# Optimization experiments

Hardware: AMD Instinct MI355X
Metric: run time of the kernel (lower is better)

The kernel has to match this reference:

```python
import jax, jax.numpy as jnp
import numpy as np

NEG = -9e15
N_NODES, IN_DIM, H1, H2, HEADS, DEC, N_EDGES, B_PAIRS = 4096, 512, 256, 128, 4, 512, 131072, 4096


def setup_inputs() -> dict:
    key = jax.random.key(0)
    ks = jax.random.split(key, 24)
    d = {}
    d["x_o"] = jax.random.normal(ks[0], (N_NODES, IN_DIM), jnp.float32)
    d["x_a"] = jax.random.normal(ks[1], (N_NODES, IN_DIM), jnp.float32)
    d["edge_index"] = jax.random.randint(ks[2], (2, N_EDGES), 0, N_NODES)
    d["idx"] = jax.random.randint(ks[3], (2, B_PAIRS), 0, N_NODES)
    # GAT layer 1 (in=IN_DIM, out=H1), per-head stacked params
    d["W1"] = jax.random.normal(ks[4], (HEADS, IN_DIM, H1)) * (IN_DIM ** -0.5)
    d["a1"] = jax.random.normal(ks[5], (HEADS, 2 * H1)) * 0.1
    d["lin1"] = jax.random.normal(ks[6], (HEADS * H1, H1)) * ((HEADS * H1) ** -0.5)
    d["res1"] = jax.random.normal(ks[7], (IN_DIM, H1)) * (IN_DIM ** -0.5)
    # GAT layer 2 (in=H1, out=H2)
    d["W2"] = jax.random.normal(ks[8], (HEADS, H1, H2)) * (H1 ** -0.5)
    d["a2"] = jax.random.normal(ks[9], (HEADS, 2 * H2)) * 0.1
    d["lin2"] = jax.random.normal(ks[10], (HEADS * H2, H2)) * ((HEADS * H2) ** -0.5)
    d["res2"] = jax.random.normal(ks[11], (H1, H2)) * (H1 ** -0.5)
    # heads
    d["mlp1_w"] = jax.random.normal(ks[12], (H2, H2)) * (H2 ** -0.5)
    d["mlp1_b"] = jnp.zeros((H2,))
    d["disc_w"] = jax.random.normal(ks[13], (H2, H2)) * (H2 ** -0.5)
    d["disc_b"] = jnp.zeros(())
    d["dec1_w"] = jax.random.normal(ks[14], (2 * H2, DEC)) * ((2 * H2) ** -0.5)
    d["dec1_b"] = jnp.zeros((DEC,))
    d["dec2_w"] = jax.random.normal(ks[15], (DEC, 1)) * (DEC ** -0.5)
    d["dec2_b"] = jnp.zeros((1,))
    d["adv_w"] = jax.random.normal(ks[16], (H2, H2)) * (H2 ** -0.5)
    d["adv_b"] = jnp.zeros((H2,))
    return d


def _gat_residual_layer(h, mask, W, a, lin, res):
    # W: [H, Fin, Fo], a: [H, 2*Fo]. e_ij = leakyrelu(Wh_i . a[:Fo] + Wh_j . a[Fo:])
    # (algebraically identical to the NxN all-pairs concat @ a in the torch code).
    def head(Wk, ak):
        Wh = h @ Wk                      # [N, Fo]
        Fo = Wk.shape[1]
        src = Wh @ ak[:Fo]               # [N]
        dst = Wh @ ak[Fo:]               # [N]
        e = jax.nn.leaky_relu(src[:, None] + dst[None, :], 0.2)  # [N, N]
        att = jax.nn.softmax(jnp.where(mask, e, NEG), axis=1)
        return jax.nn.elu(att @ Wh)      # [N, Fo]

    heads = jax.vmap(head)(W, a)         # [H, N, Fo]
    Hn, N, Fo = heads.shape
    concat = jnp.transpose(heads, (1, 0, 2)).reshape(N, Hn * Fo)
    mh = jax.nn.elu(concat @ lin)
    return jax.nn.relu(mh + h @ res)     # relu(relu(x)) == relu(x); dropout off in eval


def reference(x_o, x_a, W1, a1, lin1, res1, W2, a2, lin2, res2,
              mlp1_w, mlp1_b, disc_w, disc_b, dec1_w, dec1_b,
              dec2_w, dec2_b, adv_w, adv_b, edge_index, idx):
    N = x_o.shape[0]
    mask = jnp.zeros((N, N), jnp.bool_).at[edge_index[0], edge_index[1]].set(True)

    def encode(x):
        h = _gat_residual_layer(x, mask, W1, a1, lin1, res1)
        h = _gat_residual_layer(h, mask, W2, a2, lin2, res2)
        return h

    x2_o = encode(x_o)                   # [N, H2]
    x2_o_a = encode(x_a)

    h_os = jax.nn.sigmoid(x2_o.mean(0)) @ mlp1_w + mlp1_b      # [H2]
    h_os_a = jax.nn.sigmoid(x2_o_a.mean(0)) @ mlp1_w + mlp1_b

    def disc(c, h_pl, h_mi):  # Bilinear(h, c) with out=1
        sc1 = (h_pl @ disc_w) @ c + disc_b
        sc2 = (h_mi @ disc_w) @ c + disc_b
        return jnp.stack([sc1, sc2], axis=1)                    # [N, 2]

    ret_os = disc(h_os, x2_o, x2_o_a)
    ret_os_a = disc(h_os_a, x2_o_a, x2_o)

    # extract_entities, default branch (task_type not in {LDA, MDA, LMI})
    entity1 = x2_o[idx[0]]
    entity2 = x2_o[idx[1]]
    z = jnp.concatenate([entity1, entity2], axis=1)             # [B, 2*H2]
    hdec = jax.nn.relu(z @ dec1_w + dec1_b)
    log1 = hdec @ dec2_w + dec2_b                               # [B, 1]
    log = jax.nn.sigmoid(log1)

    sc_1 = (x2_o @ adv_w + adv_b).sum(1)[None, :]               # [1, N]
    sc_2 = (x2_o_a @ adv_w + adv_b).sum(1)[None, :]
    logits = jnp.concatenate([sc_1, sc_2], axis=1)              # [1, 2N]

    return (log, ret_os, ret_os_a, x2_o, logits, log1)
```

## Files before the change

kernel.cpp:

```cpp
#include <hip/hip_runtime.h>
#include <stdint.h>

#define N_NODES 4096
#define N_EDGES 131072

typedef __attribute__((ext_vector_type(8))) short short8;
typedef __attribute__((ext_vector_type(4))) float floatx4;

__device__ __forceinline__ float bf2f(unsigned short u) {
  union { unsigned u; float f; } v; v.u = ((unsigned)u) << 16; return v.f;
}
__device__ __forceinline__ unsigned short f2bf(float f) {
  union { float f; unsigned u; } v; v.f = f;
  unsigned r = 0x7FFFu + ((v.u >> 16) & 1u);
  return (unsigned short)((v.u + r) >> 16);
}
__device__ __forceinline__ float wredsum(float x) {
#pragma unroll
  for (int d = 32; d >= 1; d >>= 1) x += __shfl_xor(x, d);
  return x;
}
__device__ __forceinline__ float wredmax(float x) {
#pragma unroll
  for (int d = 32; d >= 1; d >>= 1) x = fmaxf(x, __shfl_xor(x, d));
  return x;
}
__device__ __forceinline__ void gload16(const void* g, void* l) {
  __builtin_amdgcn_global_load_lds(
      (const __attribute__((address_space(1))) unsigned*)g,
      (__attribute__((address_space(3))) unsigned*)l, 16, 0, 0);
}

__global__ __launch_bounds__(256) void gemm128(
    const unsigned short* __restrict__ A, const unsigned short* __restrict__ Bt,
    int M, int N, int K, unsigned short* __restrict__ Cb,
    const float* __restrict__ avec, float* __restrict__ sdv, int FO) {
  __shared__ __align__(16) unsigned short As[128 * 32];
  __shared__ __align__(16) unsigned short Bs[128 * 32];
  const int t = threadIdx.x, lane = t & 63, w = t >> 6;
  const int wr = w >> 1, wc = w & 1;
  const int n0 = blockIdx.x * 128, m0 = blockIdx.y * 128;
  floatx4 acc[4][4] = {};
  const int arow = t >> 2;
  const int schunk = (t & 3) ^ ((arow >> 1) & 3);

  for (int kt = 0; kt < K; kt += 32) {
    __syncthreads();
    gload16(A + (size_t)(m0 + arow) * K + kt + schunk * 8, &As[t * 8]);
    gload16(A + (size_t)(m0 + 64 + arow) * K + kt + schunk * 8, &As[(256 + t) * 8]);
    gload16(Bt + (size_t)(n0 + arow) * K + kt + schunk * 8, &Bs[t * 8]);
    gload16(Bt + (size_t)(n0 + 64 + arow) * K + kt + schunk * 8, &Bs[(256 + t) * 8]);
    __syncthreads();
    short8 af[4], bfr[4];
    const int koff = lane >> 4;
#pragma unroll
    for (int m = 0; m < 4; ++m) {
      const int r = wr * 64 + (lane & 15) + m * 16;
      af[m] = *(const short8*)&As[r * 32 + ((koff ^ ((r >> 1) & 3)) << 3)];
    }
#pragma unroll
    for (int n = 0; n < 4; ++n) {
      const int r = wc * 64 + (lane & 15) + n * 16;
      bfr[n] = *(const short8*)&Bs[r * 32 + ((koff ^ ((r >> 1) & 3)) << 3)];
    }
#pragma unroll
    for (int m = 0; m < 4; ++m)
#pragma unroll
      for (int n = 0; n < 4; ++n)
        acc[m][n] = __builtin_amdgcn_mfma_f32_16x16x32_bf16(af[m], bfr[n], acc[m][n], 0, 0, 0);
  }

  const int rb = m0 + wr * 64 + (lane >> 4) * 4;
  const int cb = n0 + wc * 64 + (lane & 15);
#pragma unroll
  for (int m = 0; m < 4; ++m)
#pragma unroll
    for (int n = 0; n < 4; ++n) {
      const int col = cb + n * 16;
#pragma unroll
      for (int r = 0; r < 4; ++r) {
        const int row = rb + m * 16 + r;
        Cb[(size_t)row * N + col] = f2bf(acc[m][n][r]);
      }
    }

  if (avec) {
    const int h = n0 / FO;
    const int cw0 = cb - h * FO;
    float as_[4], ad_[4];
#pragma unroll
    for (int n = 0; n < 4; ++n) {
      as_[n] = avec[h * 2 * FO + cw0 + n * 16];
      ad_[n] = avec[h * 2 * FO + FO + cw0 + n * 16];
    }
#pragma unroll
    for (int m = 0; m < 4; ++m)
#pragma unroll
      for (int r = 0; r < 4; ++r) {
        float sp = 0.f, dp = 0.f;
#pragma unroll
        for (int n = 0; n < 4; ++n) {
          sp += acc[m][n][r] * as_[n];
          dp += acc[m][n][r] * ad_[n];
        }
#pragma unroll
        for (int d = 1; d < 16; d <<= 1) {
          sp += __shfl_xor(sp, d);
          dp += __shfl_xor(dp, d);
        }
        if ((lane & 15) == 0) {
          const int row = rb + m * 16 + r;
          atomicAdd(&sdv[row * 8 + h], sp);
          atomicAdd(&sdv[row * 8 + 4 + h], dp);
        }
      }
  }
}

__device__ __forceinline__ void stage64(const unsigned short* __restrict__ G,
                                        unsigned short* lds, int row0, int K,
                                        int kt, int t) {
  const int l0 = t, l1 = t + 256;
  const int r0 = l0 >> 3, c0 = l0 & 7;
  const int r1 = l1 >> 3, c1 = l1 & 7;
  gload16(G + (size_t)(row0 + r0) * K + kt + ((c0 ^ (r0 & 7)) << 3), &lds[l0 * 8]);
  gload16(G + (size_t)(row0 + r1) * K + kt + ((c1 ^ (r1 & 7)) << 3), &lds[l1 * 8]);
}
__device__ __forceinline__ short8 frag64(const unsigned short* lds, int r, int c) {
  return *(const short8*)&lds[r * 64 + ((c ^ (r & 7)) << 3)];
}

template <int EP>
__global__ __launch_bounds__(256) void gemm64(
    const unsigned short* __restrict__ A, const unsigned short* __restrict__ Bt,
    int M, int N, int K, unsigned short* __restrict__ Cb,
    const float* __restrict__ bias) {
  __shared__ __align__(16) unsigned short As[64 * 64];
  __shared__ __align__(16) unsigned short Bs[64 * 64];
  const int t = threadIdx.x, lane = t & 63, w = t >> 6;
  const int wr = w >> 1, wc = w & 1;
  const int n0 = blockIdx.x * 64, m0 = blockIdx.y * 64;
  floatx4 acc[2][2] = {};

  for (int kt = 0; kt < K; kt += 64) {
    __syncthreads();
    stage64(A, As, m0, K, kt, t);
    stage64(Bt, Bs, n0, K, kt, t);
    __syncthreads();
    short8 af[2][2], bfv[2][2];
#pragma unroll
    for (int m = 0; m < 2; ++m) {
      const int ra = wr * 32 + (lane & 15) + m * 16;
#pragma unroll
      for (int kk = 0; kk < 2; ++kk)
        af[m][kk] = frag64(As, ra, (lane >> 4) + kk * 4);
    }
#pragma unroll
    for (int n = 0; n < 2; ++n) {
      const int rb = wc * 32 + (lane & 15) + n * 16;
#pragma unroll
      for (int kk = 0; kk < 2; ++kk)
        bfv[n][kk] = frag64(Bs, rb, (lane >> 4) + kk * 4);
    }
#pragma unroll
    for (int kk = 0; kk < 2; ++kk)
#pragma unroll
      for (int m = 0; m < 2; ++m)
#pragma unroll
        for (int n = 0; n < 2; ++n)
          acc[m][n] = __builtin_amdgcn_mfma_f32_16x16x32_bf16(af[m][kk], bfv[n][kk], acc[m][n], 0, 0, 0);
  }

  const int rb = m0 + wr * 32 + (lane >> 4) * 4;
  const int cb = n0 + wc * 32 + (lane & 15);
#pragma unroll
  for (int m = 0; m < 2; ++m)
#pragma unroll
    for (int n = 0; n < 2; ++n) {
      const int col = cb + n * 16;
#pragma unroll
      for (int r = 0; r < 4; ++r) {
        const int row = rb + m * 16 + r;
        float v = acc[m][n][r];
        if (EP == 4) { v += bias[col]; v = v > 0.f ? v : 0.f; }
        Cb[(size_t)row * N + col] = f2bf(v);
      }
    }
}

template <int EP>
__global__ __launch_bounds__(256) void gemm64dual(
    const unsigned short* __restrict__ A1, const unsigned short* __restrict__ B1t, int K1,
    const unsigned short* __restrict__ A2, const unsigned short* __restrict__ B2t, int K2,
    int N, unsigned short* __restrict__ Cb,
    float* __restrict__ Cfo, float* __restrict__ Cfa) {
  __shared__ __align__(16) unsigned short As[64 * 64];
  __shared__ __align__(16) unsigned short Bs[64 * 64];
  const int t = threadIdx.x, lane = t & 63, w = t >> 6;
  const int wr = w >> 1, wc = w & 1;
  const int n0 = blockIdx.x * 64, m0 = blockIdx.y * 64;
  floatx4 acc[2][2] = {};

#pragma unroll 1
  for (int pass = 0; pass < 2; ++pass) {
    const unsigned short* A = pass ? A2 : A1;
    const unsigned short* Bt = pass ? B2t : B1t;
    const int K = pass ? K2 : K1;
    for (int kt = 0; kt < K; kt += 64) {
      __syncthreads();
      stage64(A, As, m0, K, kt, t);
      stage64(Bt, Bs, n0, K, kt, t);
      __syncthreads();
      short8 af[2][2], bfv[2][2];
#pragma unroll
      for (int m = 0; m < 2; ++m) {
        const int ra = wr * 32 + (lane & 15) + m * 16;
#pragma unroll
        for (int kk = 0; kk < 2; ++kk)
          af[m][kk] = frag64(As, ra, (lane >> 4) + kk * 4);
      }
#pragma unroll
      for (int n = 0; n < 2; ++n) {
        const int rb = wc * 32 + (lane & 15) + n * 16;
#pragma unroll
        for (int kk = 0; kk < 2; ++kk)
          bfv[n][kk] = frag64(Bs, rb, (lane >> 4) + kk * 4);
      }
#pragma unroll
      for (int kk = 0; kk < 2; ++kk)
#pragma unroll
        for (int m = 0; m < 2; ++m)
#pragma unroll
          for (int n = 0; n < 2; ++n)
            acc[m][n] = __builtin_amdgcn_mfma_f32_16x16x32_bf16(af[m][kk], bfv[n][kk], acc[m][n], 0, 0, 0);
    }
    if (pass == 0) {
#pragma unroll
      for (int m = 0; m < 2; ++m)
#pragma unroll
        for (int n = 0; n < 2; ++n)
#pragma unroll
          for (int r = 0; r < 4; ++r) {
            float v = acc[m][n][r];
            acc[m][n][r] = v > 0.f ? v : expm1f(v);
          }
    }
  }

  const int rb = m0 + wr * 32 + (lane >> 4) * 4;
  const int cb = n0 + wc * 32 + (lane & 15);
#pragma unroll
  for (int m = 0; m < 2; ++m)
#pragma unroll
    for (int n = 0; n < 2; ++n) {
      const int col = cb + n * 16;
#pragma unroll
      for (int r = 0; r < 4; ++r) {
        const int row = rb + m * 16 + r;
        float v = acc[m][n][r];
        v = v > 0.f ? v : 0.f;
        if (EP == 0) {
          Cb[(size_t)row * N + col] = f2bf(v);
        } else {
          float* bb = (row < 4096) ? Cfo : Cfa;
          bb[(size_t)(row & 4095) * N + col] = v;
        }
      }
    }
}

__global__ __launch_bounds__(256) void scatter_kernel(
    const int* __restrict__ ei, unsigned long long* __restrict__ mb,
    float* __restrict__ sd1, float* __restrict__ sd2) {
  int b = blockIdx.x;
  if (b < 512) {
    int e = b * 256 + threadIdx.x;
    int r = ei[e], c = ei[N_EDGES + e];
    atomicOr(&mb[(size_t)r * 64 + (c >> 6)], 1ull << (c & 63));
  } else {
    int z = (b - 512) * 256 + threadIdx.x;
    if (z < 65536) sd1[z] = 0.f;
    else sd2[z - 65536] = 0.f;
  }
}

__global__ __launch_bounds__(256) void pack2_kernel(
    const float* W1, const float* lin1, const float* res1, const float* W2,
    const float* lin2, const float* res2, const float* dec1,
    const float* xo, const float* xa,
    unsigned short* dW1, unsigned short* dlin1, unsigned short* dres1,
    unsigned short* dW2, unsigned short* dlin2, unsigned short* dres2,
    unsigned short* ddec1, unsigned short* x16) {
  const int b = blockIdx.x, t = threadIdx.x;
  if (b >= 1248) {
    int ib = b - 1248;
    const float* src = (ib < 512) ? xo : xa;
    unsigned short* dst = x16 + ((ib < 512) ? 0 : (size_t)4096 * 512);
    size_t base = (size_t)(ib & 511) * 4096;
#pragma unroll
    for (int q = 0; q < 4; ++q) {
      size_t o = base + q * 1024 + t * 4;
      float4 v = *(const float4*)&src[o];
      ushort4 u = {f2bf(v.x), f2bf(v.y), f2bf(v.z), f2bf(v.w)};
      *(ushort4*)&dst[o] = u;
    }
    return;
  }
  const float* src; unsigned short* dst; int K, F, nFt, tb;
  if (b < 512)       { int h = b >> 7;        src = W1 + h * 131072; dst = dW1 + h * 131072; K = 512;  F = 256; nFt = 8;  tb = b & 127; }
  else if (b < 768)  {                        src = lin1;            dst = dlin1;            K = 1024; F = 256; nFt = 8;  tb = b - 512; }
  else if (b < 896)  {                        src = res1;            dst = dres1;            K = 512;  F = 256; nFt = 8;  tb = b - 768; }
  else if (b < 1024) { int h = (b - 896) >> 5; src = W2 + h * 32768; dst = dW2 + h * 32768;  K = 256;  F = 128; nFt = 4;  tb = (b - 896) & 31; }
  else if (b < 1088) {                        src = lin2;            dst = dlin2;            K = 512;  F = 128; nFt = 4;  tb = b - 1024; }
  else if (b < 1120) {                        src = res2;            dst = dres2;            K = 256;  F = 128; nFt = 4;  tb = b - 1088; }
  else               {                        src = dec1;            dst = ddec1;            K = 256;  F = 512; nFt = 16; tb = b - 1120; }
  const int k0 = (tb / nFt) * 32, f0 = (tb % nFt) * 32;
  __shared__ float tile[32][33];
  {
    int r = t >> 3, c4 = (t & 7) * 4;
    float4 v = *(const float4*)&src[(size_t)(k0 + r) * F + f0 + c4];
    tile[r][c4] = v.x; tile[r][c4 + 1] = v.y; tile[r][c4 + 2] = v.z; tile[r][c4 + 3] = v.w;
  }
  __syncthreads();
  {
    int f = t >> 3, k4 = (t & 7) * 4;
    ushort4 u;
    u.x = f2bf(tile[k4 + 0][f]); u.y = f2bf(tile[k4 + 1][f]);
    u.z = f2bf(tile[k4 + 2][f]); u.w = f2bf(tile[k4 + 3][f]);
    *(ushort4*)&dst[(size_t)(f0 + f) * K + k0 + k4] = u;
  }
}

template <int FO>
__global__ __launch_bounds__(256) void attn_kernel(
    const unsigned long long* __restrict__ mb, const float* __restrict__ sd,
    const unsigned short* __restrict__ Wh, unsigned short* __restrict__ outp) {
  constexpr int E = FO / 64;
  constexpr int W = 4 * FO;
  constexpr int WGCAP = 512;
  __shared__ __align__(16) char smem[8208 + 8320];
  unsigned short* nbr = (unsigned short*)smem;
  float (*wgs)[520] = (float (*)[520])(smem + 8208);
  float* red = (float*)smem;
  __shared__ int s_cnt;
  __shared__ float s_inv[4];
  const int i = blockIdx.x;
  const int mrow = i & 4095;
  const int base = i & ~4095;
  const int t = threadIdx.x;
  const int lane = t & 63, wv = t >> 6;

  if (t < 64) {
    unsigned long long wb = mb[(size_t)mrow * 64 + t];
    int pc = __popcll(wb);
    int inc = pc;
#pragma unroll
    for (int d = 1; d < 64; d <<= 1) {
      int v = __shfl_up(inc, d);
      if (t >= d) inc += v;
    }
    if (t == 63) s_cnt = inc;
    int off = inc - pc;
    while (wb) {
      int b = __builtin_ctzll(wb);
      nbr[off++] = (unsigned short)(t * 64 + b);
      wb &= wb - 1;
    }
  }
  __syncthreads();
  const int cnt = s_cnt;

  if (cnt == 0) {
    const float wg = 1.f / 4096.f;
    float acc0[E] = {};
    for (int j = 0; j < N_NODES; ++j) {
      const unsigned short* p = Wh + (size_t)(base + j) * W + wv * FO + lane * E;
#pragma unroll
      for (int q = 0; q < E; ++q) acc0[q] += wg * bf2f(p[q]);
    }
    unsigned short* op = outp + (size_t)i * W + wv * FO + lane * E;
#pragma unroll
    for (int q = 0; q < E; ++q) {
      float v = acc0[q];
      op[q] = f2bf(v > 0.f ? v : expm1f(v));
    }
    return;
  }

  if (t < 8) nbr[(cnt + t < 4103) ? cnt + t : 4103] = 0;
  const float src_i = sd[(size_t)i * 8 + wv];
  float m = -1e30f;
  for (int nn = lane; nn < cnt; nn += 64) {
    int j = base + nbr[nn];
    float x = src_i + sd[(size_t)j * 8 + 4 + wv];
    m = fmaxf(m, x > 0.f ? x : 0.2f * x);
  }
  m = wredmax(m);
  float ssum = 0.f;
  for (int nn = lane; nn < cnt; nn += 64) {
    int j = base + nbr[nn];
    float x = src_i + sd[(size_t)j * 8 + 4 + wv];
    float e = x > 0.f ? x : 0.2f * x;
    float g = __expf(e - m);
    if (nn < WGCAP) wgs[wv][nn] = g;
    ssum += g;
  }
  ssum = wredsum(ssum);
  if (lane == 0) s_inv[wv] = 1.f / ssum;
  if (lane < 8) wgs[wv][(cnt < WGCAP ? cnt : WGCAP) + lane] = 0.f;
  __syncthreads();

  float acc[4][E] = {};
  const int lim = cnt < WGCAP ? cnt : WGCAP;
  const int ngroups = (lim + 7) >> 3;
  for (int g = wv; g < ngroups; g += 4) {
    const int nn = g * 8;
    ushort4 ja = *(const ushort4*)&nbr[nn];
    ushort4 jb = *(const ushort4*)&nbr[nn + 4];
    const int js[8] = {ja.x, ja.y, ja.z, ja.w, jb.x, jb.y, jb.z, jb.w};
#pragma unroll
    for (int h = 0; h < 4; ++h) {
      float4 wa = *(const float4*)&wgs[h][nn];
      float4 wb4 = *(const float4*)&wgs[h][nn + 4];
      const float ws[8] = {wa.x, wa.y, wa.z, wa.w, wb4.x, wb4.y, wb4.z, wb4.w};
      if constexpr (E == 4) {
        uint2 r[8];
#pragma unroll
        for (int q = 0; q < 8; ++q)
          r[q] = *(const uint2*)(Wh + (size_t)(base + js[q]) * W + h * FO + lane * E);
#pragma unroll
        for (int q = 0; q < 8; ++q) {
          acc[h][0] += ws[q] * bf2f((unsigned short)(r[q].x & 0xffff));
          acc[h][1] += ws[q] * bf2f((unsigned short)(r[q].x >> 16));
          acc[h][2] += ws[q] * bf2f((unsigned short)(r[q].y & 0xffff));
          acc[h][3] += ws[q] * bf2f((unsigned short)(r[q].y >> 16));
        }
      } else {
        unsigned r[8];
#pragma unroll
        for (int q = 0; q < 8; ++q)
          r[q] = *(const unsigned*)(Wh + (size_t)(base + js[q]) * W + h * FO + lane * E);
#pragma unroll
        for (int q = 0; q < 8; ++q) {
          acc[h][0] += ws[q] * bf2f((unsigned short)(r[q] & 0xffff));
          acc[h][1] += ws[q] * bf2f((unsigned short)(r[q] >> 16));
        }
      }
    }
  }
  for (int nn = WGCAP; nn < cnt; ++nn) {
    int j = base + nbr[nn];
    float x = src_i + sd[(size_t)j * 8 + 4 + wv];
    float e = x > 0.f ? x : 0.2f * x;
    float g = __expf(e - m);
    const unsigned short* p = Wh + (size_t)j * W + wv * FO + lane * E;
#pragma unroll
    for (int q = 0; q < E; ++q) acc[wv][q] += g * bf2f(p[q]);
  }
  __syncthreads();
#pragma unroll
  for (int h = 0; h < 4; ++h)
#pragma unroll
    for (int q = 0; q < E; ++q)
      red[(wv * 4 + h) * 64 * E + lane * E + q] = acc[h][q];
  __syncthreads();
  float fin[E] = {};
#pragma unroll
  for (int w2 = 0; w2 < 4; ++w2)
#pragma unroll
    for (int q = 0; q < E; ++q)
      fin[q] += red[(w2 * 4 + wv) * 64 * E + lane * E + q];
  const float inv = s_inv[wv];
  unsigned short* op = outp + (size_t)i * W + wv * FO + lane * E;
#pragma unroll
  for (int q = 0; q < E; ++q) {
    float v = fin[q] * inv;
    op[q] = f2bf(v > 0.f ? v : expm1f(v));
  }
}

__global__ __launch_bounds__(128) void colsum_kernel(
    const float* __restrict__ x2o, const float* __restrict__ x2a,
    float* __restrict__ small) {
  int b = blockIdx.x, f = threadIdx.x;
  const float* x = (b < 64) ? x2o : x2a;
  float* s = (b < 64) ? small : (small + 128);
  int r0 = (b & 63) * 64;
  float acc = 0.f;
  for (int r = 0; r < 64; ++r) acc += x[(size_t)(r0 + r) * 128 + f];
  atomicAdd(&s[f], acc);
}

__global__ __launch_bounds__(128) void finalize_kernel(
    float* __restrict__ small, const float* __restrict__ mlp1_w,
    const float* __restrict__ mlp1_b, const float* __restrict__ disc_w,
    const float* __restrict__ adv_w, const float* __restrict__ adv_b) {
  __shared__ float so[128], sa[128], ho[128], ha[128];
  int f = threadIdx.x;
  so[f] = 1.f / (1.f + __expf(-small[f] * (1.f / 4096.f)));
  sa[f] = 1.f / (1.f + __expf(-small[128 + f] * (1.f / 4096.f)));
  __syncthreads();
  float aco = mlp1_b[f], aca = mlp1_b[f];
  for (int c = 0; c < 128; ++c) {
    aco += so[c] * mlp1_w[c * 128 + f];
    aca += sa[c] * mlp1_w[c * 128 + f];
  }
  ho[f] = aco;
  ha[f] = aca;
  __syncthreads();
  float vo = 0.f, va = 0.f, ar = 0.f;
  for (int c = 0; c < 128; ++c) {
    vo += disc_w[f * 128 + c] * ho[c];
    va += disc_w[f * 128 + c] * ha[c];
    ar += adv_w[f * 128 + c];
  }
  small[256 + f] = vo;
  small[384 + f] = va;
  small[512 + f] = ar;
  if (f == 0) {
    float b = 0.f;
    for (int c = 0; c < 128; ++c) b += adv_b[c];
    small[640] = b;
  }
}

__global__ __launch_bounds__(256) void pernode_kernel(
    const float* __restrict__ x2o, const float* __restrict__ x2a,
    const float* __restrict__ small, const float* __restrict__ disc_b,
    float* __restrict__ out) {
  const float* v_os = small + 256;
  const float* v_a = small + 384;
  const float* adv_rs = small + 512;
  int lane = threadIdx.x & 63, wv = threadIdx.x >> 6;
  int i = blockIdx.x * 4 + wv;
  float2 xo = *(const float2*)&x2o[(size_t)i * 128 + lane * 2];
  float2 xa = *(const float2*)&x2a[(size_t)i * 128 + lane * 2];
  float2 vo = *(const float2*)&v_os[lane * 2];
  float2 va = *(const float2*)&v_a[lane * 2];
  float2 ar = *(const float2*)&adv_rs[lane * 2];
  float poo = wredsum(xo.x * vo.x + xo.y * vo.y);
  float pao = wredsum(xa.x * vo.x + xa.y * vo.y);
  float paa = wredsum(xa.x * va.x + xa.y * va.y);
  float poa = wredsum(xo.x * va.x + xo.y * va.y);
  float pov = wredsum(xo.x * ar.x + xo.y * ar.y);
  float pav = wredsum(xa.x * ar.x + xa.y * ar.y);
  if (lane == 0) {
    float db = disc_b[0], bv = small[640];
    out[4096 + 2 * i] = poo + db;
    out[4096 + 2 * i + 1] = pao + db;
    out[12288 + 2 * i] = paa + db;
    out[12288 + 2 * i + 1] = poa + db;
    out[544768 + i] = pov + bv;
    out[548864 + i] = pav + bv;
  }
}

__global__ __launch_bounds__(256) void gather_kernel(
    const float* __restrict__ x2o, const int* __restrict__ idx,
    unsigned short* __restrict__ z) {
  int i = blockIdx.x, c = threadIdx.x;
  int s = (c < 128) ? idx[i] : idx[4096 + i];
  z[(size_t)i * 256 + c] = f2bf(x2o[(size_t)s * 128 + (c & 127)]);
}

__global__ __launch_bounds__(256) void dec2_kernel(
    const unsigned short* __restrict__ hdec, const float* __restrict__ w2,
    const float* __restrict__ b2, float* __restrict__ out) {
  int lane = threadIdx.x & 63, wv = threadIdx.x >> 6;
  int i = blockIdx.x * 4 + wv;
  float s = 0.f;
#pragma unroll
  for (int q = 0; q < 8; ++q) {
    int f = lane + q * 64;
    s += bf2f(hdec[(size_t)i * 512 + f]) * w2[f];
  }
  s = wredsum(s);
  if (lane == 0) {
    float v = s + b2[0];
    out[552960 + i] = v;
    out[i] = 1.f / (1.f + __expf(-v));
  }
}

extern "C" void kernel_launch(void* const* d_in, const int* in_sizes, int n_in,
                              void* d_out, int out_size, void* d_ws, size_t ws_size,
                              hipStream_t stream) {
  const float* x_o = (const float*)d_in[0];
  const float* x_a = (const float*)d_in[1];
  const int* ei = (const int*)d_in[2];
  const int* idx = (const int*)d_in[3];
  const float* W1 = (const float*)d_in[4];
  const float* a1 = (const float*)d_in[5];
  const float* lin1 = (const float*)d_in[6];
  const float* res1 = (const float*)d_in[7];
  const float* W2 = (const float*)d_in[8];
  const float* a2 = (const float*)d_in[9];
  const float* lin2 = (const float*)d_in[10];
  const float* res2 = (const float*)d_in[11];
  const float* mlp1_w = (const float*)d_in[12];
  const float* mlp1_b = (const float*)d_in[13];
  const float* disc_w = (const float*)d_in[14];
  const float* disc_b = (const float*)d_in[15];
  const float* dec1_w = (const float*)d_in[16];
  const float* dec1_b = (const float*)d_in[17];
  const float* dec2_w = (const float*)d_in[18];
  const float* dec2_b = (const float*)d_in[19];
  const float* adv_w = (const float*)d_in[20];
  const float* adv_b = (const float*)d_in[21];
  float* out = (float*)d_out;

  char* w = (char*)d_ws;
  size_t off = 0;
  auto alloc = [&](size_t b) {
    char* p = w + off;
    off += (b + 255) & ~(size_t)255;
    return p;
  };
  unsigned long long* mb = (unsigned long long*)alloc((size_t)4096 * 64 * 8);
  unsigned short* x16 = (unsigned short*)alloc((size_t)8192 * 512 * 2);
  unsigned short* Wh1 = (unsigned short*)alloc((size_t)8192 * 1024 * 2);
  unsigned short* ho1 = (unsigned short*)alloc((size_t)8192 * 1024 * 2);
  unsigned short* h1 = (unsigned short*)alloc((size_t)8192 * 256 * 2);
  unsigned short* Wh2 = (unsigned short*)alloc((size_t)8192 * 512 * 2);
  unsigned short* ho2 = (unsigned short*)alloc((size_t)8192 * 512 * 2);
  float* x2a = (float*)alloc((size_t)4096 * 128 * 4);
  float* sd1 = (float*)alloc((size_t)8192 * 8 * 4);
  float* sd2 = (float*)alloc((size_t)8192 * 8 * 4);
  float* small = (float*)alloc(1024 * 4);
  unsigned short* tW1 = (unsigned short*)alloc((size_t)524288 * 2);
  unsigned short* tlin1 = (unsigned short*)alloc((size_t)262144 * 2);
  unsigned short* tres1 = (unsigned short*)alloc((size_t)131072 * 2);
  unsigned short* tW2 = (unsigned short*)alloc((size_t)131072 * 2);
  unsigned short* tlin2 = (unsigned short*)alloc((size_t)65536 * 2);
  unsigned short* tres2 = (unsigned short*)alloc((size_t)32768 * 2);
  unsigned short* tdec1 = (unsigned short*)alloc((size_t)131072 * 2);
  unsigned short* z16 = (unsigned short*)alloc((size_t)4096 * 256 * 2);
  unsigned short* hdec = (unsigned short*)alloc((size_t)4096 * 512 * 2);

  hipMemsetAsync(mb, 0, (size_t)4096 * 64 * 8, stream);
  hipMemsetAsync(small, 0, 1024, stream);
  scatter_kernel<<<1024, 256, 0, stream>>>(ei, mb, sd1, sd2);
  pack2_kernel<<<2272, 256, 0, stream>>>(W1, lin1, res1, W2, lin2, res2, dec1_w,
                                         x_o, x_a, tW1, tlin1, tres1, tW2,
                                         tlin2, tres2, tdec1, x16);

  float* x2o_out = out + 20480;

  gemm128<<<dim3(8, 64), 256, 0, stream>>>(x16, tW1, 8192, 1024, 512, Wh1, a1, sd1, 256);
  attn_kernel<256><<<8192, 256, 0, stream>>>(mb, sd1, Wh1, ho1);
  gemm64dual<0><<<dim3(4, 128), 256, 0, stream>>>(ho1, tlin1, 1024, x16, tres1, 512, 256, h1, nullptr, nullptr);
  gemm128<<<dim3(4, 64), 256, 0, stream>>>(h1, tW2, 8192, 512, 256, Wh2, a2, sd2, 128);
  attn_kernel<128><<<8192, 256, 0, stream>>>(mb, sd2, Wh2, ho2);
  gemm64dual<1><<<dim3(2, 128), 256, 0, stream>>>(ho2, tlin2, 512, h1, tres2, 256, 128, nullptr, x2o_out, x2a);

  colsum_kernel<<<128, 128, 0, stream>>>(x2o_out, x2a, small);
  finalize_kernel<<<1, 128, 0, stream>>>(small, mlp1_w, mlp1_b, disc_w, adv_w, adv_b);
  pernode_kernel<<<1024, 256, 0, stream>>>(x2o_out, x2a, small, disc_b, out);
  gather_kernel<<<4096, 256, 0, stream>>>(x2o_out, idx, z16);
  gemm64<4><<<dim3(8, 64), 256, 0, stream>>>(z16, tdec1, 4096, 512, 256, hdec, dec1_b);
  dec2_kernel<<<1024, 256, 0, stream>>>(hdec, dec2_w, dec2_b, out);
}
```

Baseline: 232.6 us.

## Precompute CSR neighbor lists and remap attention to one wave per row-head

Adds three kernels that build a global CSR neighbor list (count, scan, fill) from the adjacency bitmask once, so the two attention layers no longer decode the bitmask per block. The attention kernel now gives each wave its own (row, head) pair, and the 8 combos of head and encoder are interleaved across blocks. This removes the cross-wave shared-memory reduction and two barriers. In exchange it adds three small launches, including a single-wave serial scan, and each wave now walks its full neighbor list alone instead of splitting the list across the block.

```diff
diff --git a/kernel.cpp b/kernel.cpp
--- a/kernel.cpp
+++ b/kernel.cpp
@@ -281,6 +281,54 @@
     int z = (b - 512) * 256 + threadIdx.x;
     if (z < 65536) sd1[z] = 0.f;
     else sd2[z - 65536] = 0.f;
+  }
+}
+
+__global__ __launch_bounds__(256) void csr_count(
+    const unsigned long long* __restrict__ mb, int* __restrict__ rcnt) {
+  int r = blockIdx.x * 256 + threadIdx.x;
+  int c = 0;
+#pragma unroll 8
+  for (int w = 0; w < 64; ++w) c += __popcll(mb[(size_t)r * 64 + w]);
+  rcnt[r] = c;
+}
+
+__global__ __launch_bounds__(64) void csr_scan(
+    const int* __restrict__ rcnt, int* __restrict__ rbase) {
+  int l = threadIdx.x;
+  int s = 0;
+  for (int k = 0; k < 64; ++k) s += rcnt[l * 64 + k];
+  int pre = s;
+#pragma unroll
+  for (int d = 1; d < 64; d <<= 1) {
+    int v = __shfl_up(pre, d);
+    if (l >= d) pre += v;
+  }
+  pre -= s;
+  int run = pre;
+  for (int k = 0; k < 64; ++k) {
+    rbase[l * 64 + k] = run;
+    run += rcnt[l * 64 + k];
+  }
+}
+
+__global__ __launch_bounds__(64) void csr_fill(
+    const unsigned long long* __restrict__ mb, const int* __restrict__ rbase,
+    unsigned short* __restrict__ nbrg) {
+  int r = blockIdx.x, t = threadIdx.x;
+  unsigned long long wb = mb[(size_t)r * 64 + t];
+  int pc = __popcll(wb);
+  int inc = pc;
+#pragma unroll
+  for (int d = 1; d < 64; d <<= 1) {
+    int v = __shfl_up(inc, d);
+    if (t >= d) inc += v;
+  }
+  int off = rbase[r] + inc - pc;
+  while (wb) {
+    int b = __builtin_ctzll(wb);
+    nbrg[off++] = (unsigned short)(t * 64 + b);
+    wb &= wb - 1;
   }
 }
 
@@ -332,149 +380,103 @@
 }
 
 template <int FO>
-__global__ __launch_bounds__(256) void attn_kernel(
-    const unsigned long long* __restrict__ mb, const float* __restrict__ sd,
+__global__ __launch_bounds__(256) void attn2_kernel(
+    const int* __restrict__ rcnt, const int* __restrict__ rbase,
+    const unsigned short* __restrict__ nbrg, const float* __restrict__ sd,
     const unsigned short* __restrict__ Wh, unsigned short* __restrict__ outp) {
   constexpr int E = FO / 64;
   constexpr int W = 4 * FO;
-  constexpr int WGCAP = 512;
-  __shared__ __align__(16) char smem[8208 + 8320];
-  unsigned short* nbr = (unsigned short*)smem;
-  float (*wgs)[520] = (float (*)[520])(smem + 8208);
-  float* red = (float*)smem;
-  __shared__ int s_cnt;
-  __shared__ float s_inv[4];
-  const int i = blockIdx.x;
-  const int mrow = i & 4095;
-  const int base = i & ~4095;
-  const int t = threadIdx.x;
-  const int lane = t & 63, wv = t >> 6;
-
-  if (t < 64) {
-    unsigned long long wb = mb[(size_t)mrow * 64 + t];
-    int pc = __popcll(wb);
-    int inc = pc;
-#pragma unroll
-    for (int d = 1; d < 64; d <<= 1) {
-      int v = __shfl_up(inc, d);
-      if (t >= d) inc += v;
-    }
-    if (t == 63) s_cnt = inc;
-    int off = inc - pc;
-    while (wb) {
-      int b = __builtin_ctzll(wb);
-      nbr[off++] = (unsigned short)(t * 64 + b);
-      wb &= wb - 1;
-    }
-  }
-  __syncthreads();
-  const int cnt = s_cnt;
-
-  if (cnt == 0) {
-    const float wg = 1.f / 4096.f;
-    float acc0[E] = {};
-    for (int j = 0; j < N_NODES; ++j) {
-      const unsigned short* p = Wh + (size_t)(base + j) * W + wv * FO + lane * E;
-#pragma unroll
-      for (int q = 0; q < E; ++q) acc0[q] += wg * bf2f(p[q]);
-    }
-    unsigned short* op = outp + (size_t)i * W + wv * FO + lane * E;
-#pragma unroll
-    for (int q = 0; q < E; ++q) {
-      float v = acc0[q];
-      op[q] = f2bf(v > 0.f ? v : expm1f(v));
-    }
-    return;
-  }
-
-  if (t < 8) nbr[(cnt + t < 4103) ? cnt + t : 4103] = 0;
-  const float src_i = sd[(size_t)i * 8 + wv];
-  float m = -1e30f;
-  for (int nn = lane; nn < cnt; nn += 64) {
-    int j = base + nbr[nn];
-    float x = src_i + sd[(size_t)j * 8 + 4 + wv];
-    m = fmaxf(m, x > 0.f ? x : 0.2f * x);
-  }
-  m = wredmax(m);
-  float ssum = 0.f;
-  for (int nn = lane; nn < cnt; nn += 64) {
-    int j = base + nbr[nn];
-    float x = src_i + sd[(size_t)j * 8 + 4 + wv];
-    float e = x > 0.f ? x : 0.2f * x;
-    float g = __expf(e - m);
-    if (nn < WGCAP) wgs[wv][nn] = g;
-    ssum += g;
-  }
-  ssum = wredsum(ssum);
-  if (lane == 0) s_inv[wv] = 1.f / ssum;
-  if (lane < 8) wgs[wv][(cnt < WGCAP ? cnt : WGCAP) + lane] = 0.f;
-  __syncthreads();
-
-  float acc[4][E] = {};
-  const int lim = cnt < WGCAP ? cnt : WGCAP;
-  const int ngroups = (lim + 7) >> 3;
-  for (int g = wv; g < ngroups; g += 4) {
-    const int nn = g * 8;
-    ushort4 ja = *(const ushort4*)&nbr[nn];
-    ushort4 jb = *(const ushort4*)&nbr[nn + 4];
-    const int js[8] = {ja.x, ja.y, ja.z, ja.w, jb.x, jb.y, jb.z, jb.w};
-#pragma unroll
-    for (int h = 0; h < 4; ++h) {
-      float4 wa = *(const float4*)&wgs[h][nn];
-      float4 wb4 = *(const float4*)&wgs[h][nn + 4];
+  constexpr int CAP = 512;
+  __shared__ __align__(16) unsigned short nb[4][CAP + 8];
+  __shared__ __align__(16) float wg[4][CAP + 8];
+  const int bid = blockIdx.x;
+  const int combo = bid & 7, chunk = bid >> 3;
+  const int h = combo & 3, e = combo >> 2;
+  const int t = threadIdx.x, lane = t & 63, wv = t >> 6;
+  const int r = chunk * 4 + wv;
+  const int i = e * 4096 + r;
+  const int jb = e * 4096;
+  const int cnt = rcnt[r], boff = rbase[r];
+  const float src_i = sd[(size_t)i * 8 + h];
+  float acc[E] = {};
+  float inv = 1.f;
+
+  if (cnt > 0) {
+    float m = -1e30f;
+    for (int nn = lane; nn < cnt; nn += 64) {
+      int j = nbrg[boff + nn];
+      if (nn < CAP) nb[wv][nn] = (unsigned short)j;
+      float x = src_i + sd[(size_t)(jb + j) * 8 + 4 + h];
+      m = fmaxf(m, x > 0.f ? x : 0.2f * x);
+    }
+    m = wredmax(m);
+    float ssum = 0.f;
+    for (int nn = lane; nn < cnt; nn += 64) {
+      int j = nbrg[boff + nn];
+      float x = src_i + sd[(size_t)(jb + j) * 8 + 4 + h];
+      float ee = x > 0.f ? x : 0.2f * x;
+      float g = __expf(ee - m);
+      if (nn < CAP) wg[wv][nn] = g;
+      ssum += g;
+    }
+    ssum = wredsum(ssum);
+    inv = 1.f / ssum;
+    const int limc = cnt < CAP ? cnt : CAP;
+    if (lane < 8) { nb[wv][limc + lane] = 0; wg[wv][limc + lane] = 0.f; }
+    const int ngroups = (limc + 7) >> 3;
+    for (int g = 0; g < ngroups; ++g) {
+      const int nn = g * 8;
+      ushort4 ja = *(const ushort4*)&nb[wv][nn];
+      ushort4 jb4 = *(const ushort4*)&nb[wv][nn + 4];
+      float4 wa = *(const float4*)&wg[wv][nn];
+      float4 wb4 = *(const float4*)&wg[wv][nn + 4];
+      const int js[8] = {ja.x, ja.y, ja.z, ja.w, jb4.x, jb4.y, jb4.z, jb4.w};
       const float ws[8] = {wa.x, wa.y, wa.z, wa.w, wb4.x, wb4.y, wb4.z, wb4.w};
       if constexpr (E == 4) {
-        uint2 r[8];
+        uint2 rv[8];
 #pragma unroll
         for (int q = 0; q < 8; ++q)
-          r[q] = *(const uint2*)(Wh + (size_t)(base + js[q]) * W + h * FO + lane * E);
+          rv[q] = *(const uint2*)(Wh + (size_t)(jb + js[q]) * W + h * FO + lane * 4);
 #pragma unroll
         for (int q = 0; q < 8; ++q) {
-          acc[h][0] += ws[q] * bf2f((unsigned short)(r[q].x & 0xffff));
-          acc[h][1] += ws[q] * bf2f((unsigned short)(r[q].x >> 16));
-          acc[h][2] += ws[q] * bf2f((unsigned short)(r[q].y & 0xffff));
-          acc[h][3] += ws[q] * bf2f((unsigned short)(r[q].y >> 16));
+          acc[0] += ws[q] * bf2f((unsigned short)(rv[q].x & 0xffff));
+          acc[1] += ws[q] * bf2f((unsigned short)(rv[q].x >> 16));
+          acc[2] += ws[q] * bf2f((unsigned short)(rv[q].y & 0xffff));
+          acc[3] += ws[q] * bf2f((unsigned short)(rv[q].y >> 16));
         }
       } else {
-        unsigned r[8];
+        unsigned rv[8];
 #pragma unroll
         for (int q = 0; q < 8; ++q)
-          r[q] = *(const unsigned*)(Wh + (size_t)(base + js[q]) * W + h * FO + lane * E);
+          rv[q] = *(const unsigned*)(Wh + (size_t)(jb + js[q]) * W + h * FO + lane * 2);
 #pragma unroll
         for (int q = 0; q < 8; ++q) {
-          acc[h][0] += ws[q] * bf2f((unsigned short)(r[q] & 0xffff));
-          acc[h][1] += ws[q] * bf2f((unsigned short)(r[q] >> 16));
+          acc[0] += ws[q] * bf2f((unsigned short)(rv[q] & 0xffff));
+          acc[1] += ws[q] * bf2f((unsigned short)(rv[q] >> 16));
         }
       }
     }
-  }
-  for (int nn = WGCAP; nn < cnt; ++nn) {
-    int j = base + nbr[nn];
-    float x = src_i + sd[(size_t)j * 8 + 4 + wv];
-    float e = x > 0.f ? x : 0.2f * x;
-    float g = __expf(e - m);
-    const unsigned short* p = Wh + (size_t)j * W + wv * FO + lane * E;
-#pragma unroll
-    for (int q = 0; q < E; ++q) acc[wv][q] += g * bf2f(p[q]);
-  }
-  __syncthreads();
-#pragma unroll
-  for (int h = 0; h < 4; ++h)
-#pragma unroll
-    for (int q = 0; q < E; ++q)
-      red[(wv * 4 + h) * 64 * E + lane * E + q] = acc[h][q];
-  __syncthreads();
-  float fin[E] = {};
-#pragma unroll
-  for (int w2 = 0; w2 < 4; ++w2)
-#pragma unroll
-    for (int q = 0; q < E; ++q)
-      fin[q] += red[(w2 * 4 + wv) * 64 * E + lane * E + q];
-  const float inv = s_inv[wv];
-  unsigned short* op = outp + (size_t)i * W + wv * FO + lane * E;
+    for (int nn = CAP; nn < cnt; ++nn) {
+      int j = nbrg[boff + nn];
+      float x = src_i + sd[(size_t)(jb + j) * 8 + 4 + h];
+      float ee = x > 0.f ? x : 0.2f * x;
+      float g = __expf(ee - m);
+      const unsigned short* p = Wh + (size_t)(jb + j) * W + h * FO + lane * E;
+#pragma unroll
+      for (int q = 0; q < E; ++q) acc[q] += g * bf2f(p[q]);
+    }
+  } else {
+    const float wgu = 1.f / 4096.f;
+    for (int j = 0; j < N_NODES; ++j) {
+      const unsigned short* p = Wh + (size_t)(jb + j) * W + h * FO + lane * E;
+#pragma unroll
+      for (int q = 0; q < E; ++q) acc[q] += wgu * bf2f(p[q]);
+    }
+  }
+  unsigned short* op = outp + (size_t)i * W + h * FO + lane * E;
 #pragma unroll
   for (int q = 0; q < E; ++q) {
-    float v = fin[q] * inv;
+    float v = acc[q] * inv;
     op[q] = f2bf(v > 0.f ? v : expm1f(v));
   }
 }
@@ -627,6 +629,9 @@
   float* sd1 = (float*)alloc((size_t)8192 * 8 * 4);
   float* sd2 = (float*)alloc((size_t)8192 * 8 * 4);
   float* small = (float*)alloc(1024 * 4);
+  int* rcnt = (int*)alloc(4096 * 4);
+  int* rbase = (int*)alloc(4096 * 4);
+  unsigned short* nbrg = (unsigned short*)alloc((size_t)(N_EDGES + 64) * 2);
   unsigned short* tW1 = (unsigned short*)alloc((size_t)524288 * 2);
   unsigned short* tlin1 = (unsigned short*)alloc((size_t)262144 * 2);
   unsigned short* tres1 = (unsigned short*)alloc((size_t)131072 * 2);
@@ -643,14 +648,17 @@
   pack2_kernel<<<2272, 256, 0, stream>>>(W1, lin1, res1, W2, lin2, res2, dec1_w,
                                          x_o, x_a, tW1, tlin1, tres1, tW2,
                                          tlin2, tres2, tdec1, x16);
+  csr_count<<<16, 256, 0, stream>>>(mb, rcnt);
+  csr_scan<<<1, 64, 0, stream>>>(rcnt, rbase);
+  csr_fill<<<4096, 64, 0, stream>>>(mb, rbase, nbrg);
 
   float* x2o_out = out + 20480;
 
   gemm128<<<dim3(8, 64), 256, 0, stream>>>(x16, tW1, 8192, 1024, 512, Wh1, a1, sd1, 256);
-  attn_kernel<256><<<8192, 256, 0, stream>>>(mb, sd1, Wh1, ho1);
+  attn2_kernel<256><<<8192, 256, 0, stream>>>(rcnt, rbase, nbrg, sd1, Wh1, ho1);
   gemm64dual<0><<<dim3(4, 128), 256, 0, stream>>>(ho1, tlin1, 1024, x16, tres1, 512, 256, h1, nullptr, nullptr);
   gemm128<<<dim3(4, 64), 256, 0, stream>>>(h1, tW2, 8192, 512, 256, Wh2, a2, sd2, 128);
-  attn_kernel<128><<<8192, 256, 0, stream>>>(mb, sd2, Wh2, ho2);
+  attn2_kernel<128><<<8192, 256, 0, stream>>>(rcnt, rbase, nbrg, sd2, Wh2, ho2);
   gemm64dual<1><<<dim3(2, 128), 256, 0, stream>>>(ho2, tlin2, 512, h1, tres2, 256, 128, nullptr, x2o_out, x2a);
 
   colsum_kernel<<<128, 128, 0, stream>>>(x2o_out, x2a, small);
```

After: 229.6 us. No clear change (-1.3%).
